# Performance work log

Hardware: AMD Instinct MI355X
Metric: run time of the kernel (lower is better)

## Reference

```python
import jax, jax.numpy as jnp
import numpy as np

N, E, IN, HID, OUT = 100000, 1600000, 128, 128, 64


def setup_inputs() -> dict:
    key = jax.random.key(0)
    k1, k2, k3, k4 = jax.random.split(key, 4)
    x = jax.random.normal(k1, (N, IN), dtype=jnp.float32)
    edge_index = jax.random.randint(k2, (2, E), 0, N, dtype=jnp.int64)
    W1 = jax.random.normal(k3, (IN, HID), dtype=jnp.float32) * (1.0 / np.sqrt(IN))
    b1 = jnp.zeros((HID,), dtype=jnp.float32)
    W2 = jax.random.normal(k4, (HID, OUT), dtype=jnp.float32) * (1.0 / np.sqrt(HID))
    b2 = jnp.zeros((OUT,), dtype=jnp.float32)
    return {"x": x, "edge_index": edge_index, "W1": W1, "b1": b1, "W2": W2, "b2": b2}


def _gcn_conv(x, src, dst, norm, W, b):
    # linear transform first (PyG order when reducing feature dim), then SpMM
    h = x @ W                                   # [N, F_out]
    msg = h[src] * norm[:, None]                # [E+N, F_out] gathered messages
    out = jax.ops.segment_sum(msg, dst, num_segments=x.shape[0])
    return out + b


def _norm_coeffs(edge_index, num_nodes, dtype):
    # add self-loops and compute symmetric normalization deg^-1/2[src]*deg^-1/2[dst]
    loop = jnp.arange(num_nodes, dtype=edge_index.dtype)
    src = jnp.concatenate([edge_index[0], loop])
    dst = jnp.concatenate([edge_index[1], loop])
    deg = jax.ops.segment_sum(jnp.ones_like(dst, dtype=dtype), dst, num_segments=num_nodes)
    dinv = jnp.where(deg > 0, jax.lax.rsqrt(jnp.maximum(deg, 1.0)), 0.0)
    norm = dinv[src] * dinv[dst]
    return src, dst, norm


def reference(x, edge_index, W1, b1, W2, b2):
    # eval-mode forward: dropout is identity
    src, dst, norm = _norm_coeffs(edge_index, x.shape[0], x.dtype)
    h = jax.nn.relu(_gcn_conv(x, src, dst, norm, W1, b1))
    out = _gcn_conv(h, src, dst, norm, W2, b2)
    return out
```

## Files before the change

### kernel.cpp

```cpp
#include <hip/hip_runtime.h>
#include <hip/hip_bf16.h>

#define DEVINL __device__ __forceinline__

DEVINL int clampidx(int v, int n) { return ((unsigned)v < (unsigned)n) ? v : 0; }
DEVINL float bflo(unsigned int u) { return __uint_as_float(u << 16); }
DEVINL float bfhi(unsigned int u) { return __uint_as_float(u & 0xffff0000u); }
DEVINL unsigned int f2bf(float f) {
    unsigned int u = __float_as_uint(f);
    u += 0x7fffu + ((u >> 16) & 1u);
    return u >> 16;
}

__global__ __launch_bounds__(256) void k_bktscan(const int* __restrict__ bktCnt,
                                                 int* __restrict__ bktBase,
                                                 int* __restrict__ bktCur, int NB) {
    __shared__ int sh[256];
    int carry = 0;
    for (int c0 = 0; c0 < NB; c0 += 256) {
        const int i = c0 + threadIdx.x;
        const int v = (i < NB) ? bktCnt[i] : 0;
        sh[threadIdx.x] = v;
        __syncthreads();
        for (int off = 1; off < 256; off <<= 1) {
            int t = (threadIdx.x >= off) ? sh[threadIdx.x - off] : 0;
            __syncthreads();
            sh[threadIdx.x] += t;
            __syncthreads();
        }
        if (i < NB) {
            const int excl = carry + sh[threadIdx.x] - v;
            bktBase[i] = excl;
            bktCur[i] = excl;
        }
        const int tot = sh[255];
        __syncthreads();
        carry += tot;
    }
    if (threadIdx.x == 0) bktBase[NB] = carry;
}

__global__ __launch_bounds__(256) void k_bktscatter(const int* __restrict__ ei,
                                                    int* __restrict__ bktCur,
                                                    unsigned int* __restrict__ packed,
                                                    int E, int n) {
    __shared__ unsigned int sPack[4096];
    __shared__ unsigned short sBkt[4096];
    __shared__ int sHist[1024], sStart[1024], sLoc[1024];
    for (int i = threadIdx.x; i < 1024; i += 256) {
        sHist[i] = 0;
        sLoc[i] = 0;
    }
    __syncthreads();
    const int base = blockIdx.x * 4096;
#pragma unroll
    for (int j = 0; j < 16; ++j) {
        const int k = j * 256 + threadIdx.x;
        const int i = base + k;
        if (i < E) {
            const int s = clampidx(ei[i], n);
            const int d = clampidx(ei[(size_t)E + i], n);
            const int b = d >> 7;
            sPack[k] = ((unsigned)(d & 127) << 25) | (unsigned)s;
            sBkt[k] = (unsigned short)b;
            atomicAdd(&sHist[b], 1);
        }
    }
    __syncthreads();
    for (int b = threadIdx.x; b < 1024; b += 256) {
        const int c = sHist[b];
        sStart[b] = c ? atomicAdd(&bktCur[b], c) : 0;
    }
    __syncthreads();
#pragma unroll
    for (int j = 0; j < 16; ++j) {
        const int k = j * 256 + threadIdx.x;
        const int i = base + k;
        if (i < E) {
            const int b = sBkt[k];
            const int pos = sStart[b] + atomicAdd(&sLoc[b], 1);
            packed[pos] = sPack[k];
        }
    }
}

__global__ __launch_bounds__(256) void k_bktfill(const unsigned int* __restrict__ packed,
                                                 const int* __restrict__ bktBase,
                                                 int* __restrict__ p, float* __restrict__ dinv,
                                                 int* __restrict__ srcs, int n) {
    constexpr int CAP = 8192;
    __shared__ unsigned int sPack[CAP];
    __shared__ int sSrc[CAP];
    __shared__ int deg[128], incl[128], cur[128];
    const int bkt = blockIdx.x;
    const int e0 = bktBase[bkt], e1 = bktBase[bkt + 1];
    const int cnt = e1 - e0;
    const int tid = threadIdx.x;
    if (tid < 128) deg[tid] = 0;
    __syncthreads();
    for (int i = tid; i < cnt; i += 256) {
        const unsigned int u = packed[e0 + i];
        if (i < CAP) sPack[i] = u;
        atomicAdd(&deg[u >> 25], 1);
    }
    __syncthreads();
    if (tid < 128) incl[tid] = deg[tid];
    __syncthreads();
    for (int off = 1; off < 128; off <<= 1) {
        const int v = (tid < 128 && tid >= off) ? incl[tid - off] : 0;
        __syncthreads();
        if (tid < 128) incl[tid] += v;
        __syncthreads();
    }
    const int node0 = bkt << 7;
    if (tid < 128) {
        cur[tid] = incl[tid] - deg[tid];
        const int node = node0 + tid;
        if (node < n) {
            p[node] = e0 + incl[tid];
            dinv[node] = rsqrtf((float)deg[tid] + 1.0f);
        }
    }
    __syncthreads();
    for (int i = tid; i < cnt; i += 256) {
        const unsigned int u = (i < CAP) ? sPack[i] : packed[e0 + i];
        const int dl = (int)(u >> 25);
        const int s = (int)(u & 0x1FFFFFFu);
        const int pos = atomicAdd(&cur[dl], 1);
        if (pos < CAP) sSrc[pos] = s;
        else srcs[e0 + pos] = s;
    }
    __syncthreads();
    const int lim = cnt < CAP ? cnt : CAP;
    for (int i = tid; i < lim; i += 256) srcs[e0 + i] = sSrc[i];
}

template <int BCOLS, bool IN_BF16>
DEVINL void gemm_body(const void* __restrict__ Xv, const float* __restrict__ W,
                      unsigned int* __restrict__ Y, int ystrideU, int n, int blk,
                      float* Ws, float* xs) {
    constexpr int KC = 32;
    constexpr int CG = BCOLS / 8;
    constexpr int RG = 256 / CG;
    constexpr int BROWS = RG * 4;
    constexpr int P = BROWS + 4;

    const int tid = threadIdx.x;
    const int row0 = blk * BROWS;
    const int ct = tid % CG;
    const int rt = tid / CG;

    float acc[4][8];
#pragma unroll
    for (int i = 0; i < 4; ++i)
#pragma unroll
        for (int j = 0; j < 8; ++j) acc[i][j] = 0.0f;

    for (int k0 = 0; k0 < 128; k0 += KC) {
        __syncthreads();
        for (int idx = tid * 4; idx < KC * BCOLS; idx += 1024)
            *(float4*)&Ws[idx] = *(const float4*)&W[(size_t)k0 * BCOLS + idx];
        if (IN_BF16) {
            const int row = tid >> 1, q = tid & 1;
            const int grow = row0 + row;
            const unsigned int* src =
                (const unsigned int*)Xv + (size_t)grow * 64 + (k0 >> 1) + q * 8;
            uint4 u0 = make_uint4(0, 0, 0, 0), u1 = make_uint4(0, 0, 0, 0);
            if (grow < n) {
                u0 = *(const uint4*)src;
                u1 = *(const uint4*)(src + 4);
            }
            const int kb = q * 16;
            float* xp = &xs[row];
            xp[(kb + 0) * P] = bflo(u0.x); xp[(kb + 1) * P] = bfhi(u0.x);
            xp[(kb + 2) * P] = bflo(u0.y); xp[(kb + 3) * P] = bfhi(u0.y);
            xp[(kb + 4) * P] = bflo(u0.z); xp[(kb + 5) * P] = bfhi(u0.z);
            xp[(kb + 6) * P] = bflo(u0.w); xp[(kb + 7) * P] = bfhi(u0.w);
            xp[(kb + 8) * P] = bflo(u1.x); xp[(kb + 9) * P] = bfhi(u1.x);
            xp[(kb + 10) * P] = bflo(u1.y); xp[(kb + 11) * P] = bfhi(u1.y);
            xp[(kb + 12) * P] = bflo(u1.z); xp[(kb + 13) * P] = bfhi(u1.z);
            xp[(kb + 14) * P] = bflo(u1.w); xp[(kb + 15) * P] = bfhi(u1.w);
        } else {
            const int row = tid >> 2, q = tid & 3;
            const int grow = row0 + row;
            const float* src = (const float*)Xv + (size_t)grow * 128 + k0 + q * 8;
            float4 v0 = make_float4(0, 0, 0, 0), v1 = make_float4(0, 0, 0, 0);
            if (grow < n) {
                v0 = *(const float4*)src;
                v1 = *(const float4*)(src + 4);
            }
            const int kb = q * 8;
            float* xp = &xs[row];
            xp[(kb + 0) * P] = v0.x; xp[(kb + 1) * P] = v0.y;
            xp[(kb + 2) * P] = v0.z; xp[(kb + 3) * P] = v0.w;
            xp[(kb + 4) * P] = v1.x; xp[(kb + 5) * P] = v1.y;
            xp[(kb + 6) * P] = v1.z; xp[(kb + 7) * P] = v1.w;
        }
        __syncthreads();

#pragma unroll 8
        for (int k = 0; k < KC; ++k) {
            const float4 xv = *(const float4*)&xs[k * P + rt * 4];
            const float4 wA = *(const float4*)&Ws[k * BCOLS + ct * 8];
            const float4 wB = *(const float4*)&Ws[k * BCOLS + ct * 8 + 4];
            const float xr[4] = {xv.x, xv.y, xv.z, xv.w};
#pragma unroll
            for (int i = 0; i < 4; ++i) {
                acc[i][0] = fmaf(xr[i], wA.x, acc[i][0]);
                acc[i][1] = fmaf(xr[i], wA.y, acc[i][1]);
                acc[i][2] = fmaf(xr[i], wA.z, acc[i][2]);
                acc[i][3] = fmaf(xr[i], wA.w, acc[i][3]);
                acc[i][4] = fmaf(xr[i], wB.x, acc[i][4]);
                acc[i][5] = fmaf(xr[i], wB.y, acc[i][5]);
                acc[i][6] = fmaf(xr[i], wB.z, acc[i][6]);
                acc[i][7] = fmaf(xr[i], wB.w, acc[i][7]);
            }
        }
    }

#pragma unroll
    for (int i = 0; i < 4; ++i) {
        const int row = row0 + rt * 4 + i;
        if (row < n) {
            uint4 o;
            o.x = f2bf(acc[i][0]) | (f2bf(acc[i][1]) << 16);
            o.y = f2bf(acc[i][2]) | (f2bf(acc[i][3]) << 16);
            o.z = f2bf(acc[i][4]) | (f2bf(acc[i][5]) << 16);
            o.w = f2bf(acc[i][6]) | (f2bf(acc[i][7]) << 16);
            *(uint4*)&Y[(size_t)row * ystrideU + ct * 4] = o;
        }
    }
}

__global__ __launch_bounds__(256) void k_gemm64(const void* __restrict__ Xv,
                                                const float* __restrict__ W,
                                                unsigned int* __restrict__ Y, int ystrideU,
                                                int n) {
    __shared__ float Ws[32 * 64];
    __shared__ float xs[32 * 132];
    gemm_body<64, true>(Xv, W, Y, ystrideU, n, blockIdx.x, Ws, xs);
}

__global__ __launch_bounds__(256) void k_gemm128_count(const void* __restrict__ Xv,
                                                       const float* __restrict__ W,
                                                       unsigned int* __restrict__ Y, int n,
                                                       const int* __restrict__ ei,
                                                       int* __restrict__ bktCnt, int E,
                                                       int nCnt) {
    __shared__ float Ws[32 * 128];
    __shared__ float xs[32 * 68];
    if ((int)blockIdx.x < nCnt) {
        int* hist = (int*)Ws;
        for (int i = threadIdx.x; i < 1024; i += 256) hist[i] = 0;
        __syncthreads();
        const int base = blockIdx.x * 4096;
#pragma unroll
        for (int j = 0; j < 16; ++j) {
            int i = base + j * 256 + threadIdx.x;
            if (i < E) atomicAdd(&hist[clampidx(ei[(size_t)E + i], n) >> 7], 1);
        }
        __syncthreads();
        for (int b = threadIdx.x; b < 1024; b += 256) {
            int c = hist[b];
            if (c) atomicAdd(&bktCnt[b], c);
        }
    } else {
        gemm_body<128, false>(Xv, W, Y, 64, n, (int)blockIdx.x - nCnt, Ws, xs);
    }
}

__global__ __launch_bounds__(256) void k_gather128(const unsigned int* __restrict__ XW,
                                                   const int* __restrict__ p,
                                                   const int* __restrict__ srcs,
                                                   const float* __restrict__ dinv,
                                                   const float* __restrict__ b1,
                                                   unsigned int* __restrict__ H1b, int n) {
    const int node = __builtin_amdgcn_readfirstlane(blockIdx.x * 4 + (threadIdx.x >> 6));
    if (node >= n) return;
    const int t = threadIdx.x & 63;
    const int start = (node == 0) ? 0 : p[node - 1];
    const int end = p[node];
    const float din = dinv[node];
    const unsigned int us = XW[(size_t)node * 64 + t];
    float a0 = bflo(us) * din, a1 = bfhi(us) * din;

    int c = start;
    for (; c + 16 <= end; c += 16) {
        int s[16];
#pragma unroll
        for (int k = 0; k < 16; ++k) s[k] = __builtin_amdgcn_readfirstlane(srcs[c + k]);
        float w[16];
        unsigned int u[16];
#pragma unroll
        for (int k = 0; k < 16; ++k) {
            w[k] = dinv[s[k]];
            u[k] = XW[((unsigned)s[k] << 6) + t];
        }
#pragma unroll
        for (int k = 0; k < 16; ++k) {
            a0 = fmaf(bflo(u[k]), w[k], a0);
            a1 = fmaf(bfhi(u[k]), w[k], a1);
        }
    }
    for (; c + 4 <= end; c += 4) {
        int s[4];
#pragma unroll
        for (int k = 0; k < 4; ++k) s[k] = __builtin_amdgcn_readfirstlane(srcs[c + k]);
        float w[4];
        unsigned int u[4];
#pragma unroll
        for (int k = 0; k < 4; ++k) {
            w[k] = dinv[s[k]];
            u[k] = XW[((unsigned)s[k] << 6) + t];
        }
#pragma unroll
        for (int k = 0; k < 4; ++k) {
            a0 = fmaf(bflo(u[k]), w[k], a0);
            a1 = fmaf(bfhi(u[k]), w[k], a1);
        }
    }
    for (; c < end; ++c) {
        const int s = __builtin_amdgcn_readfirstlane(srcs[c]);
        const float w = dinv[s];
        const unsigned int u = XW[((unsigned)s << 6) + t];
        a0 = fmaf(bflo(u), w, a0);
        a1 = fmaf(bfhi(u), w, a1);
    }
    const float r0 = fmaxf(fmaf(a0, din, b1[2 * t]), 0.0f);
    const float r1 = fmaxf(fmaf(a1, din, b1[2 * t + 1]), 0.0f);
    H1b[(size_t)node * 64 + t] = f2bf(r0) | (f2bf(r1) << 16);
}

__global__ __launch_bounds__(256) void k_gather64(const unsigned short* __restrict__ h2,
                                                  const int* __restrict__ p,
                                                  const int* __restrict__ srcs,
                                                  const float* __restrict__ dinv,
                                                  const float* __restrict__ b2,
                                                  float* __restrict__ out, int n) {
    const int node = __builtin_amdgcn_readfirstlane(blockIdx.x * 4 + (threadIdx.x >> 6));
    if (node >= n) return;
    const int t = threadIdx.x & 63;
    const int start = (node == 0) ? 0 : p[node - 1];
    const int end = p[node];
    const float din = dinv[node];
    float acc = bflo(h2[(size_t)node * 64 + t]) * din;

    int c = start;
    for (; c + 16 <= end; c += 16) {
        int s[16];
#pragma unroll
        for (int k = 0; k < 16; ++k) s[k] = __builtin_amdgcn_readfirstlane(srcs[c + k]);
        float w[16], v[16];
#pragma unroll
        for (int k = 0; k < 16; ++k) {
            w[k] = dinv[s[k]];
            v[k] = bflo(h2[((unsigned)s[k] << 6) + t]);
        }
#pragma unroll
        for (int k = 0; k < 16; ++k) acc = fmaf(v[k], w[k], acc);
    }
    for (; c + 4 <= end; c += 4) {
        int s[4];
#pragma unroll
        for (int k = 0; k < 4; ++k) s[k] = __builtin_amdgcn_readfirstlane(srcs[c + k]);
        float w[4], v[4];
#pragma unroll
        for (int k = 0; k < 4; ++k) {
            w[k] = dinv[s[k]];
            v[k] = bflo(h2[((unsigned)s[k] << 6) + t]);
        }
#pragma unroll
        for (int k = 0; k < 4; ++k) acc = fmaf(v[k], w[k], acc);
    }
    for (; c < end; ++c) {
        const int s = __builtin_amdgcn_readfirstlane(srcs[c]);
        const float w = dinv[s];
        acc = fmaf(bflo(h2[((unsigned)s << 6) + t]), w, acc);
    }
    out[(size_t)node * 64 + t] = fmaf(acc, din, b2[t]);
}

extern "C" void kernel_launch(void* const* d_in, const int* in_sizes, int n_in,
                              void* d_out, int out_size, void* d_ws, size_t ws_size,
                              hipStream_t stream) {
    const float* x  = (const float*)d_in[0];
    const int* ei   = (const int*)d_in[1];
    const float* W1 = (const float*)d_in[2];
    const float* b1 = (const float*)d_in[3];
    const float* W2 = (const float*)d_in[4];
    const float* b2 = (const float*)d_in[5];

    const int n = in_sizes[0] / 128;
    const int E = in_sizes[1] / 2;
    const int NB = (n + 127) >> 7;

    auto al = [](size_t b) { return (b + 255) & ~(size_t)255; };
    const size_t off_p    = 0;
    const size_t off_dinv = off_p + al((size_t)n * 4);
    const size_t off_srcs = off_dinv + al((size_t)n * 4);
    const size_t off_XW   = off_srcs + al((size_t)E * 4);
    const size_t off_H1b  = off_XW + al((size_t)n * 64 * 4);
    const size_t need     = off_H1b + (size_t)n * 64 * 4;
    const size_t off_pk   = off_H1b;
    const size_t off_bc   = off_pk + al((size_t)E * 4);
    const size_t off_bb   = off_bc + al(1024 * 4);
    const size_t off_bu   = off_bb + al(1025 * 4);

    if (ws_size < need || NB > 1024) {
        hipMemsetAsync(d_out, 0, (size_t)out_size * 4, stream);
        return;
    }

    int*          p    = (int*)((char*)d_ws + off_p);
    float*        dinv = (float*)((char*)d_ws + off_dinv);
    int*          srcs = (int*)((char*)d_ws + off_srcs);
    unsigned int* XW   = (unsigned int*)((char*)d_ws + off_XW);
    unsigned int* H1b  = (unsigned int*)((char*)d_ws + off_H1b);
    unsigned int* pk   = (unsigned int*)((char*)d_ws + off_pk);
    int*          bCnt = (int*)((char*)d_ws + off_bc);
    int*          bBase= (int*)((char*)d_ws + off_bb);
    int*          bCur = (int*)((char*)d_ws + off_bu);
    float*        out  = (float*)d_out;

    const int gEdge = (E + 4095) / 4096;
    const int gGemm = (n + 63) / 64;
    const int gG    = (n + 3) / 4;

    hipMemsetAsync(bCnt, 0, 1024 * 4, stream);
    k_gemm128_count<<<gEdge + gGemm, 256, 0, stream>>>(x, W1, XW, n, ei, bCnt, E, gEdge);

    k_bktscan<<<1, 256, 0, stream>>>(bCnt, bBase, bCur, NB);
    k_bktscatter<<<gEdge, 256, 0, stream>>>(ei, bCur, pk, E, n);
    k_bktfill<<<NB, 256, 0, stream>>>(pk, bBase, p, dinv, srcs, n);

    k_gather128<<<gG, 256, 0, stream>>>(XW, p, srcs, dinv, b1, H1b, n);

    k_gemm64<<<(n + 127) / 128, 256, 0, stream>>>(H1b, W2, XW, 32, n);

    k_gather64<<<gG, 256, 0, stream>>>((const unsigned short*)XW, p, srcs, dinv, b2, out, n);
}
```

Before: 351.0 us.

## Replace FP32 SIMT GEMMs with split-bf16 MFMA matrix-core GEMMs

Both dense transforms (x@W1 and H1@W2) move from shared-memory FP32 FMA tiling to MFMA 16x16x32 bf16 instructions. To keep accuracy near FP32, inputs and weights are split into hi/lo bf16 parts and combined with three (or two) MFMAs per tile. A small prep kernel transposes and splits the weights into the workspace. The cost is extra MFMA work, one more launch, and uncoalesced 2-byte output stores. Operands are read directly from global memory without shared-memory staging.

```diff
diff --git a/kernel.cpp b/kernel.cpp
--- a/kernel.cpp
+++ b/kernel.cpp
@@ -2,6 +2,14 @@
 #include <hip/hip_bf16.h>
 
 #define DEVINL __device__ __forceinline__
+
+typedef __attribute__((ext_vector_type(8))) short bf16x8;
+typedef __attribute__((ext_vector_type(4))) float f32x4;
+
+union U8 {
+    bf16x8 v;
+    uint4 u;
+};
 
 DEVINL int clampidx(int v, int n) { return ((unsigned)v < (unsigned)n) ? v : 0; }
 DEVINL float bflo(unsigned int u) { return __uint_as_float(u << 16); }
@@ -10,6 +18,46 @@
     unsigned int u = __float_as_uint(f);
     u += 0x7fffu + ((u >> 16) & 1u);
     return u >> 16;
+}
+
+DEVINL void split8(const float4 v0, const float4 v1, uint4& hi, uint4& lo) {
+    const float xv[8] = {v0.x, v0.y, v0.z, v0.w, v1.x, v1.y, v1.z, v1.w};
+    unsigned h[8], l[8];
+#pragma unroll
+    for (int j = 0; j < 8; ++j) {
+        h[j] = f2bf(xv[j]);
+        const float r = xv[j] - bflo(h[j]);
+        l[j] = f2bf(r);
+    }
+    hi = make_uint4(h[0] | (h[1] << 16), h[2] | (h[3] << 16),
+                    h[4] | (h[5] << 16), h[6] | (h[7] << 16));
+    lo = make_uint4(l[0] | (l[1] << 16), l[2] | (l[3] << 16),
+                    l[4] | (l[5] << 16), l[6] | (l[7] << 16));
+}
+
+__global__ __launch_bounds__(256) void k_wprep(const float* __restrict__ W1,
+                                               const float* __restrict__ W2,
+                                               unsigned short* __restrict__ WT1h,
+                                               unsigned short* __restrict__ WT1l,
+                                               unsigned short* __restrict__ WT2h,
+                                               unsigned short* __restrict__ WT2l) {
+    const int i = blockIdx.x * 256 + threadIdx.x;
+    if (i < 16384) {
+        const int nn = i & 127, k = i >> 7;
+        const float v = W1[k * 128 + nn];
+        const unsigned h = f2bf(v);
+        const float r = v - bflo(h);
+        WT1h[nn * 128 + k] = (unsigned short)h;
+        WT1l[nn * 128 + k] = (unsigned short)f2bf(r);
+    }
+    if (i < 8192) {
+        const int nn = i & 63, k = i >> 6;
+        const float v = W2[k * 64 + nn];
+        const unsigned h = f2bf(v);
+        const float r = v - bflo(h);
+        WT2h[nn * 128 + k] = (unsigned short)h;
+        WT2l[nn * 128 + k] = (unsigned short)f2bf(r);
+    }
 }
 
 __global__ __launch_bounds__(256) void k_bktscan(const int* __restrict__ bktCnt,
@@ -135,122 +183,12 @@
     for (int i = tid; i < lim; i += 256) srcs[e0 + i] = sSrc[i];
 }
 
-template <int BCOLS, bool IN_BF16>
-DEVINL void gemm_body(const void* __restrict__ Xv, const float* __restrict__ W,
-                      unsigned int* __restrict__ Y, int ystrideU, int n, int blk,
-                      float* Ws, float* xs) {
-    constexpr int KC = 32;
-    constexpr int CG = BCOLS / 8;
-    constexpr int RG = 256 / CG;
-    constexpr int BROWS = RG * 4;
-    constexpr int P = BROWS + 4;
-
-    const int tid = threadIdx.x;
-    const int row0 = blk * BROWS;
-    const int ct = tid % CG;
-    const int rt = tid / CG;
-
-    float acc[4][8];
-#pragma unroll
-    for (int i = 0; i < 4; ++i)
-#pragma unroll
-        for (int j = 0; j < 8; ++j) acc[i][j] = 0.0f;
-
-    for (int k0 = 0; k0 < 128; k0 += KC) {
-        __syncthreads();
-        for (int idx = tid * 4; idx < KC * BCOLS; idx += 1024)
-            *(float4*)&Ws[idx] = *(const float4*)&W[(size_t)k0 * BCOLS + idx];
-        if (IN_BF16) {
-            const int row = tid >> 1, q = tid & 1;
-            const int grow = row0 + row;
-            const unsigned int* src =
-                (const unsigned int*)Xv + (size_t)grow * 64 + (k0 >> 1) + q * 8;
-            uint4 u0 = make_uint4(0, 0, 0, 0), u1 = make_uint4(0, 0, 0, 0);
-            if (grow < n) {
-                u0 = *(const uint4*)src;
-                u1 = *(const uint4*)(src + 4);
-            }
-            const int kb = q * 16;
-            float* xp = &xs[row];
-            xp[(kb + 0) * P] = bflo(u0.x); xp[(kb + 1) * P] = bfhi(u0.x);
-            xp[(kb + 2) * P] = bflo(u0.y); xp[(kb + 3) * P] = bfhi(u0.y);
-            xp[(kb + 4) * P] = bflo(u0.z); xp[(kb + 5) * P] = bfhi(u0.z);
-            xp[(kb + 6) * P] = bflo(u0.w); xp[(kb + 7) * P] = bfhi(u0.w);
-            xp[(kb + 8) * P] = bflo(u1.x); xp[(kb + 9) * P] = bfhi(u1.x);
-            xp[(kb + 10) * P] = bflo(u1.y); xp[(kb + 11) * P] = bfhi(u1.y);
-            xp[(kb + 12) * P] = bflo(u1.z); xp[(kb + 13) * P] = bfhi(u1.z);
-            xp[(kb + 14) * P] = bflo(u1.w); xp[(kb + 15) * P] = bfhi(u1.w);
-        } else {
-            const int row = tid >> 2, q = tid & 3;
-            const int grow = row0 + row;
-            const float* src = (const float*)Xv + (size_t)grow * 128 + k0 + q * 8;
-            float4 v0 = make_float4(0, 0, 0, 0), v1 = make_float4(0, 0, 0, 0);
-            if (grow < n) {
-                v0 = *(const float4*)src;
-                v1 = *(const float4*)(src + 4);
-            }
-            const int kb = q * 8;
-            float* xp = &xs[row];
-            xp[(kb + 0) * P] = v0.x; xp[(kb + 1) * P] = v0.y;
-            xp[(kb + 2) * P] = v0.z; xp[(kb + 3) * P] = v0.w;
-            xp[(kb + 4) * P] = v1.x; xp[(kb + 5) * P] = v1.y;
-            xp[(kb + 6) * P] = v1.z; xp[(kb + 7) * P] = v1.w;
-        }
-        __syncthreads();
-
-#pragma unroll 8
-        for (int k = 0; k < KC; ++k) {
-            const float4 xv = *(const float4*)&xs[k * P + rt * 4];
-            const float4 wA = *(const float4*)&Ws[k * BCOLS + ct * 8];
-            const float4 wB = *(const float4*)&Ws[k * BCOLS + ct * 8 + 4];
-            const float xr[4] = {xv.x, xv.y, xv.z, xv.w};
-#pragma unroll
-            for (int i = 0; i < 4; ++i) {
-                acc[i][0] = fmaf(xr[i], wA.x, acc[i][0]);
-                acc[i][1] = fmaf(xr[i], wA.y, acc[i][1]);
-                acc[i][2] = fmaf(xr[i], wA.z, acc[i][2]);
-                acc[i][3] = fmaf(xr[i], wA.w, acc[i][3]);
-                acc[i][4] = fmaf(xr[i], wB.x, acc[i][4]);
-                acc[i][5] = fmaf(xr[i], wB.y, acc[i][5]);
-                acc[i][6] = fmaf(xr[i], wB.z, acc[i][6]);
-                acc[i][7] = fmaf(xr[i], wB.w, acc[i][7]);
-            }
-        }
-    }
-
-#pragma unroll
-    for (int i = 0; i < 4; ++i) {
-        const int row = row0 + rt * 4 + i;
-        if (row < n) {
-            uint4 o;
-            o.x = f2bf(acc[i][0]) | (f2bf(acc[i][1]) << 16);
-            o.y = f2bf(acc[i][2]) | (f2bf(acc[i][3]) << 16);
-            o.z = f2bf(acc[i][4]) | (f2bf(acc[i][5]) << 16);
-            o.w = f2bf(acc[i][6]) | (f2bf(acc[i][7]) << 16);
-            *(uint4*)&Y[(size_t)row * ystrideU + ct * 4] = o;
-        }
-    }
-}
-
-__global__ __launch_bounds__(256) void k_gemm64(const void* __restrict__ Xv,
-                                                const float* __restrict__ W,
-                                                unsigned int* __restrict__ Y, int ystrideU,
-                                                int n) {
-    __shared__ float Ws[32 * 64];
-    __shared__ float xs[32 * 132];
-    gemm_body<64, true>(Xv, W, Y, ystrideU, n, blockIdx.x, Ws, xs);
-}
-
-__global__ __launch_bounds__(256) void k_gemm128_count(const void* __restrict__ Xv,
-                                                       const float* __restrict__ W,
-                                                       unsigned int* __restrict__ Y, int n,
-                                                       const int* __restrict__ ei,
-                                                       int* __restrict__ bktCnt, int E,
-                                                       int nCnt) {
-    __shared__ float Ws[32 * 128];
-    __shared__ float xs[32 * 68];
+__global__ __launch_bounds__(256) void k_gemm1_count(
+    const float* __restrict__ x, const unsigned short* __restrict__ WTh,
+    const unsigned short* __restrict__ WTl, unsigned short* __restrict__ Y16, int n,
+    const int* __restrict__ ei, int* __restrict__ bktCnt, int E, int nCnt) {
+    __shared__ int hist[1024];
     if ((int)blockIdx.x < nCnt) {
-        int* hist = (int*)Ws;
         for (int i = threadIdx.x; i < 1024; i += 256) hist[i] = 0;
         __syncthreads();
         const int base = blockIdx.x * 4096;
@@ -264,8 +202,110 @@
             int c = hist[b];
             if (c) atomicAdd(&bktCnt[b], c);
         }
+        return;
+    }
+    const int blk = (int)blockIdx.x - nCnt;
+    const int lane = threadIdx.x & 63;
+    const int row16 = lane & 15;
+    const int kg = lane >> 4;
+    const int rowbase = blk * 64 + (threadIdx.x >> 6) * 16;
+    const int grow = rowbase + row16;
+
+    U8 ahi[4], alo[4];
+    if (grow < n) {
+        const float* xp = x + (size_t)grow * 128 + kg * 8;
+#pragma unroll
+        for (int k0 = 0; k0 < 4; ++k0) {
+            const float4 v0 = *(const float4*)(xp + k0 * 32);
+            const float4 v1 = *(const float4*)(xp + k0 * 32 + 4);
+            split8(v0, v1, ahi[k0].u, alo[k0].u);
+        }
     } else {
-        gemm_body<128, false>(Xv, W, Y, 64, n, (int)blockIdx.x - nCnt, Ws, xs);
+#pragma unroll
+        for (int k0 = 0; k0 < 4; ++k0) {
+            ahi[k0].u = make_uint4(0, 0, 0, 0);
+            alo[k0].u = make_uint4(0, 0, 0, 0);
+        }
+    }
+
+    f32x4 acc[8];
+#pragma unroll
+    for (int nt = 0; nt < 8; ++nt) acc[nt] = (f32x4){0.f, 0.f, 0.f, 0.f};
+
+#pragma unroll
+    for (int nt = 0; nt < 8; ++nt) {
+        const unsigned short* bp = WTh + (size_t)(nt * 16 + row16) * 128 + kg * 8;
+        const unsigned short* bq = WTl + (size_t)(nt * 16 + row16) * 128 + kg * 8;
+#pragma unroll
+        for (int k0 = 0; k0 < 4; ++k0) {
+            U8 bh, bl;
+            bh.u = *(const uint4*)(bp + k0 * 32);
+            bl.u = *(const uint4*)(bq + k0 * 32);
+            acc[nt] = __builtin_amdgcn_mfma_f32_16x16x32_bf16(ahi[k0].v, bh.v, acc[nt], 0, 0, 0);
+            acc[nt] = __builtin_amdgcn_mfma_f32_16x16x32_bf16(alo[k0].v, bh.v, acc[nt], 0, 0, 0);
+            acc[nt] = __builtin_amdgcn_mfma_f32_16x16x32_bf16(ahi[k0].v, bl.v, acc[nt], 0, 0, 0);
+        }
+    }
+
+    const int m4 = (lane >> 4) * 4;
+#pragma unroll
+    for (int nt = 0; nt < 8; ++nt) {
+#pragma unroll
+        for (int r = 0; r < 4; ++r) {
+            const int orow = rowbase + m4 + r;
+            if (orow < n)
+                Y16[(size_t)orow * 128 + nt * 16 + row16] = (unsigned short)f2bf(acc[nt][r]);
+        }
+    }
+}
+
+__global__ __launch_bounds__(256) void k_gemm2_mfma(const unsigned short* __restrict__ H16,
+                                                    const unsigned short* __restrict__ WTh,
+                                                    const unsigned short* __restrict__ WTl,
+                                                    unsigned short* __restrict__ Y16, int n) {
+    const int lane = threadIdx.x & 63;
+    const int row16 = lane & 15;
+    const int kg = lane >> 4;
+    const int rowbase = blockIdx.x * 64 + (threadIdx.x >> 6) * 16;
+    const int grow = rowbase + row16;
+
+    U8 a[4];
+    if (grow < n) {
+        const unsigned short* ap = H16 + (size_t)grow * 128 + kg * 8;
+#pragma unroll
+        for (int k0 = 0; k0 < 4; ++k0) a[k0].u = *(const uint4*)(ap + k0 * 32);
+    } else {
+#pragma unroll
+        for (int k0 = 0; k0 < 4; ++k0) a[k0].u = make_uint4(0, 0, 0, 0);
+    }
+
+    f32x4 acc[4];
+#pragma unroll
+    for (int nt = 0; nt < 4; ++nt) acc[nt] = (f32x4){0.f, 0.f, 0.f, 0.f};
+
+#pragma unroll
+    for (int nt = 0; nt < 4; ++nt) {
+        const unsigned short* bp = WTh + (size_t)(nt * 16 + row16) * 128 + kg * 8;
+        const unsigned short* bq = WTl + (size_t)(nt * 16 + row16) * 128 + kg * 8;
+#pragma unroll
+        for (int k0 = 0; k0 < 4; ++k0) {
+            U8 bh, bl;
+            bh.u = *(const uint4*)(bp + k0 * 32);
+            bl.u = *(const uint4*)(bq + k0 * 32);
+            acc[nt] = __builtin_amdgcn_mfma_f32_16x16x32_bf16(a[k0].v, bh.v, acc[nt], 0, 0, 0);
+            acc[nt] = __builtin_amdgcn_mfma_f32_16x16x32_bf16(a[k0].v, bl.v, acc[nt], 0, 0, 0);
+        }
+    }
+
+    const int m4 = (lane >> 4) * 4;
+#pragma unroll
+    for (int nt = 0; nt < 4; ++nt) {
+#pragma unroll
+        for (int r = 0; r < 4; ++r) {
+            const int orow = rowbase + m4 + r;
+            if (orow < n)
+                Y16[(size_t)orow * 64 + nt * 16 + row16] = (unsigned short)f2bf(acc[nt][r]);
+        }
     }
 }
 
@@ -400,7 +440,11 @@
     const size_t off_srcs = off_dinv + al((size_t)n * 4);
     const size_t off_XW   = off_srcs + al((size_t)E * 4);
     const size_t off_H1b  = off_XW + al((size_t)n * 64 * 4);
-    const size_t need     = off_H1b + (size_t)n * 64 * 4;
+    const size_t off_w1h  = off_H1b + al((size_t)n * 64 * 4);
+    const size_t off_w1l  = off_w1h + al(128 * 128 * 2);
+    const size_t off_w2h  = off_w1l + al(128 * 128 * 2);
+    const size_t off_w2l  = off_w2h + al(64 * 128 * 2);
+    const size_t need     = off_w2l + (size_t)64 * 128 * 2;
     const size_t off_pk   = off_H1b;
     const size_t off_bc   = off_pk + al((size_t)E * 4);
     const size_t off_bb   = off_bc + al(1024 * 4);
@@ -411,23 +455,30 @@
         return;
     }
 
-    int*          p    = (int*)((char*)d_ws + off_p);
-    float*        dinv = (float*)((char*)d_ws + off_dinv);
-    int*          srcs = (int*)((char*)d_ws + off_srcs);
-    unsigned int* XW   = (unsigned int*)((char*)d_ws + off_XW);
-    unsigned int* H1b  = (unsigned int*)((char*)d_ws + off_H1b);
-    unsigned int* pk   = (unsigned int*)((char*)d_ws + off_pk);
-    int*          bCnt = (int*)((char*)d_ws + off_bc);
-    int*          bBase= (int*)((char*)d_ws + off_bb);
-    int*          bCur = (int*)((char*)d_ws + off_bu);
-    float*        out  = (float*)d_out;
+    int*            p    = (int*)((char*)d_ws + off_p);
+    float*          dinv = (float*)((char*)d_ws + off_dinv);
+    int*            srcs = (int*)((char*)d_ws + off_srcs);
+    unsigned int*   XW   = (unsigned int*)((char*)d_ws + off_XW);
+    unsigned int*   H1b  = (unsigned int*)((char*)d_ws + off_H1b);
+    unsigned int*   pk   = (unsigned int*)((char*)d_ws + off_pk);
+    int*            bCnt = (int*)((char*)d_ws + off_bc);
+    int*            bBase= (int*)((char*)d_ws + off_bb);
+    int*            bCur = (int*)((char*)d_ws + off_bu);
+    unsigned short* WT1h = (unsigned short*)((char*)d_ws + off_w1h);
+    unsigned short* WT1l = (unsigned short*)((char*)d_ws + off_w1l);
+    unsigned short* WT2h = (unsigned short*)((char*)d_ws + off_w2h);
+    unsigned short* WT2l = (unsigned short*)((char*)d_ws + off_w2l);
+    float*          out  = (float*)d_out;
 
     const int gEdge = (E + 4095) / 4096;
-    const int gGemm = (n + 63) / 64;
+    const int gM    = (n + 63) / 64;
     const int gG    = (n + 3) / 4;
 
     hipMemsetAsync(bCnt, 0, 1024 * 4, stream);
-    k_gemm128_count<<<gEdge + gGemm, 256, 0, stream>>>(x, W1, XW, n, ei, bCnt, E, gEdge);
+    k_wprep<<<64, 256, 0, stream>>>(W1, W2, WT1h, WT1l, WT2h, WT2l);
+
+    k_gemm1_count<<<gEdge + gM, 256, 0, stream>>>(x, WT1h, WT1l, (unsigned short*)XW, n,
+                                                  ei, bCnt, E, gEdge);
 
     k_bktscan<<<1, 256, 0, stream>>>(bCnt, bBase, bCur, NB);
     k_bktscatter<<<gEdge, 256, 0, stream>>>(ei, bCur, pk, E, n);
@@ -435,7 +486,8 @@
 
     k_gather128<<<gG, 256, 0, stream>>>(XW, p, srcs, dinv, b1, H1b, n);
 
-    k_gemm64<<<(n + 127) / 128, 256, 0, stream>>>(H1b, W2, XW, 32, n);
+    k_gemm2_mfma<<<gM, 256, 0, stream>>>((const unsigned short*)H1b, WT2h, WT2l,
+                                         (unsigned short*)XW, n);
 
     k_gather64<<<gG, 256, 0, stream>>>((const unsigned short*)XW, p, srcs, dinv, b2, out, n);
 }
```

Measured after the change: 354.1 us. No clear change (+0.9%).
